# Kernel optimization log

Measured on AMD Instinct MI355X. Metric: run time of the kernel, lower is better.

## Reference

```python
import jax, jax.numpy as jnp
import numpy as np

C_Z = 128
C_S = 1024
C_S_OUT = 1024
B, L = 1, 1024


def setup_inputs() -> dict:
    key = jax.random.key(0)
    ks = jax.random.split(key, 8)
    s_z = jax.random.normal(ks[0], (B, L, L, C_Z), dtype=jnp.float32)
    s_s_in = jax.random.normal(ks[1], (B, L, C_S), dtype=jnp.float32)
    pair_mask = jnp.ones((B, L, L), dtype=jnp.float32)
    scale = 0.02
    return {
        "s_z": s_z,
        "s_s_in": s_s_in,
        "pair_mask": pair_mask,
        "ln_g": jnp.ones((C_Z,), jnp.float32),
        "ln_b": jnp.zeros((C_Z,), jnp.float32),
        "w1": jax.random.normal(ks[2], (C_Z, C_Z), jnp.float32) * scale,
        "b1": jnp.zeros((C_Z,), jnp.float32),
        "w2": jax.random.normal(ks[3], (C_Z, C_Z), jnp.float32) * scale,
        "b2": jnp.zeros((C_Z,), jnp.float32),
        "wc": jax.random.normal(ks[4], (C_S_OUT, 2 * C_Z + C_S), jnp.float32) * scale,
        "bc": jnp.zeros((C_S_OUT,), jnp.float32),
    }


def _layernorm(x, g, b, eps=1e-5):
    mu = jnp.mean(x, axis=-1, keepdims=True)
    var = jnp.mean(jnp.square(x - mu), axis=-1, keepdims=True)
    return (x - mu) * jax.lax.rsqrt(var + eps) * g + b


def reference(s_z, s_s_in, pair_mask, ln_g, ln_b, w1, b1, w2, b2, wc, bc):
    # LayerNorm -> Linear -> ReLU -> Linear over last dim (c_z)
    z = _layernorm(s_z, ln_g, ln_b)
    z = jax.nn.relu(jnp.einsum("blmc,dc->blmd", z, w1) + b1)
    z = jnp.einsum("blmc,dc->blmd", z, w2) + b2
    z = z * pair_mask[..., None]
    # masked mean over columns (dim=2) and rows (dim=1)
    norm_c = jnp.clip(jnp.sum(pair_mask, axis=2), 1.0, None)  # (B, L)
    s_s_c = jnp.sum(z, axis=2) / norm_c[..., None]            # (B, L, c_z)
    norm_r = jnp.clip(jnp.sum(pair_mask, axis=1), 1.0, None)
    s_s_r = jnp.sum(z, axis=1) / norm_r[..., None]
    cat = jnp.concatenate([s_s_c, s_s_r, s_s_in], axis=-1)    # (B, L, 2*c_z + c_s)
    return jnp.einsum("blc,dc->bld", cat, wc) + bc            # (B, L, c_s_out)
```

## Files before the change

kernel.cpp:

```cpp
#include <hip/hip_runtime.h>
#include <hip/hip_bf16.h>


typedef short bf16x8 __attribute__((ext_vector_type(8)));
typedef short short4v __attribute__((ext_vector_type(4)));
typedef float f32x16 __attribute__((ext_vector_type(16)));

static __device__ __forceinline__ short f2bf(float f) {
  unsigned u = __float_as_uint(f);
  u += 0x7fffu + ((u >> 16) & 1u);
  return (short)(u >> 16);
}
static __device__ __forceinline__ float bf2f(short s) {
  return __uint_as_float(((unsigned)(unsigned short)s) << 16);
}

__global__ __launch_bounds__(256, 2) void k_pair(
    const float* __restrict__ z, const float* __restrict__ pm,
    const float* __restrict__ lng, const float* __restrict__ lnb,
    const float* __restrict__ w1, const float* __restrict__ b1,
    float* __restrict__ g, float* __restrict__ gr,
    float* __restrict__ Mc, float* __restrict__ Mr)
{
  __shared__ __align__(16) short As[2][64 * 136];
  __shared__ float maskS[2][64];

  const int tid  = threadIdx.x;
  const int lane = tid & 63;
  const int wv   = tid >> 6;
  const int rt   = wv >> 1;
  const int ch   = wv & 1;
  const int ln   = lane & 31;
  const int hh   = lane >> 5;
  const int l0   = blockIdx.y * 32;
  const int m0   = blockIdx.x * 32;
  const int c8   = (tid & 15) * 8;

  float lg[8], lb[8];
  #pragma unroll
  for (int j = 0; j < 8; ++j) { lg[j] = lng[c8 + j]; lb[j] = lnb[c8 + j]; }

  float b1v[2];
  #pragma unroll
  for (int cc = 0; cc < 2; ++cc) b1v[cc] = b1[(ch * 2 + cc) * 32 + ln];

  bf16x8 bF[2][8];
  #pragma unroll
  for (int cc = 0; cc < 2; ++cc) {
    const int n = (ch * 2 + cc) * 32 + ln;
    #pragma unroll
    for (int k0 = 0; k0 < 8; ++k0) {
      const float* wp = w1 + n * 128 + k0 * 16 + hh * 8;
      float4 f0 = *(const float4*)wp;
      float4 f1 = *(const float4*)(wp + 4);
      bf16x8 t;
      t[0]=f2bf(f0.x); t[1]=f2bf(f0.y); t[2]=f2bf(f0.z); t[3]=f2bf(f0.w);
      t[4]=f2bf(f1.x); t[5]=f2bf(f1.y); t[6]=f2bf(f1.z); t[7]=f2bf(f1.w);
      bF[cc][k0] = t;
    }
  }

  float grA[2][16];
  #pragma unroll
  for (int cc = 0; cc < 2; ++cc)
    #pragma unroll
    for (int i = 0; i < 16; ++i) grA[cc][i] = 0.f;
  float mrAcc = 0.f;

  float4 xa[4], xb[4];
  float  mv = 0.f;
  auto LOADB = [&](int b) {
    #pragma unroll
    for (int p = 0; p < 4; ++p) {
      const int r = p * 16 + (tid >> 4);
      const int l = l0 + b * 2 + (r >> 5);
      const int m = m0 + (r & 31);
      const float* src = z + ((size_t)l * 1024 + (size_t)m) * 128 + c8;
      xa[p] = *(const float4*)src;
      xb[p] = *(const float4*)(src + 4);
    }
    if (tid < 64)
      mv = pm[(size_t)(l0 + b * 2 + (tid >> 5)) * 1024 + (m0 + (tid & 31))];
  };

  LOADB(0);

  #pragma unroll 1
  for (int b = 0; b < 16; ++b) {
    const int buf = b & 1;
    #pragma unroll
    for (int p = 0; p < 4; ++p) {
      const int r = p * 16 + (tid >> 4);
      float x[8] = {xa[p].x, xa[p].y, xa[p].z, xa[p].w,
                    xb[p].x, xb[p].y, xb[p].z, xb[p].w};
      float s = 0.f, s2 = 0.f;
      #pragma unroll
      for (int j = 0; j < 8; ++j) { s += x[j]; s2 += x[j] * x[j]; }
      #pragma unroll
      for (int off = 1; off < 16; off <<= 1) {
        s  += __shfl_xor(s, off);
        s2 += __shfl_xor(s2, off);
      }
      const float mu  = s * (1.f / 128.f);
      const float var = s2 * (1.f / 128.f) - mu * mu;
      const float rs  = rsqrtf(var + 1e-5f);
      bf16x8 o;
      #pragma unroll
      for (int j = 0; j < 8; ++j) o[j] = f2bf((x[j] - mu) * rs * lg[j] + lb[j]);
      *(bf16x8*)(&As[buf][r * 136 + c8]) = o;
    }
    if (tid < 64) maskS[buf][tid] = mv;
    __syncthreads();

    if (b < 15) LOADB(b + 1);

    f32x16 acc0, acc1;
    #pragma unroll
    for (int i = 0; i < 16; ++i) { acc0[i] = 0.f; acc1[i] = 0.f; }
    #pragma unroll
    for (int k0 = 0; k0 < 8; ++k0) {
      bf16x8 aF = *(bf16x8*)(&As[buf][(rt * 32 + ln) * 136 + k0 * 16 + hh * 8]);
      acc0 = __builtin_amdgcn_mfma_f32_32x32x16_bf16(aF, bF[0][k0], acc0, 0, 0, 0);
      acc1 = __builtin_amdgcn_mfma_f32_32x32x16_bf16(aF, bF[1][k0], acc1, 0, 0, 0);
    }

    float mrow[16];
    #pragma unroll
    for (int i = 0; i < 16; ++i) {
      const int cr = (i & 3) + 8 * (i >> 2) + 4 * hh;
      mrow[i] = maskS[buf][rt * 32 + cr];
    }
    const int lrow = l0 + b * 2 + rt;
    float s0 = 0.f, s1 = 0.f;
    #pragma unroll
    for (int i = 0; i < 16; ++i) {
      const float v0 = fmaxf(acc0[i] + b1v[0], 0.f) * mrow[i];
      const float v1 = fmaxf(acc1[i] + b1v[1], 0.f) * mrow[i];
      grA[0][i] += v0; grA[1][i] += v1;
      s0 += v0; s1 += v1;
    }
    s0 += __shfl_xor(s0, 32);
    s1 += __shfl_xor(s1, 32);
    if (lane < 32) {
      atomicAdd(&g[lrow * 128 + (ch * 2 + 0) * 32 + lane], s0);
      atomicAdd(&g[lrow * 128 + (ch * 2 + 1) * 32 + lane], s1);
    }

    if (wv == 0) {
      const float v = maskS[buf][lane];
      mrAcc += v;
      float rsum = v;
      #pragma unroll
      for (int off = 1; off < 32; off <<= 1) rsum += __shfl_xor(rsum, off);
      if (ln == 0) atomicAdd(&Mc[l0 + b * 2 + hh], rsum);
    }
  }

  if (wv == 0) {
    const float v = mrAcc + __shfl_xor(mrAcc, 32);
    if (lane < 32) atomicAdd(&Mr[m0 + lane], v);
  }

  __syncthreads();
  float* red1 = (float*)&As[0][0];
  if (rt == 1) {
    #pragma unroll
    for (int cc = 0; cc < 2; ++cc)
      #pragma unroll
      for (int i = 0; i < 16; ++i) {
        const int cr = (i & 3) + 8 * (i >> 2) + 4 * hh;
        red1[((ch * 2 + cc) * 32 + cr) * 32 + ln] = grA[cc][i];
      }
  }
  __syncthreads();
  if (rt == 0) {
    #pragma unroll
    for (int cc = 0; cc < 2; ++cc)
      #pragma unroll
      for (int i = 0; i < 16; ++i) {
        const int cr = (i & 3) + 8 * (i >> 2) + 4 * hh;
        const float v = grA[cc][i] + red1[((ch * 2 + cc) * 32 + cr) * 32 + ln];
        atomicAdd(&gr[(m0 + cr) * 128 + (ch * 2 + cc) * 32 + ln], v);
      }
  }
}

__global__ __launch_bounds__(256, 2) void k_seqproj(
    const float* __restrict__ gg, const float* __restrict__ w2,
    const float* __restrict__ b2, const float* __restrict__ Mc,
    const float* __restrict__ Mr, short* __restrict__ Ah, short* __restrict__ Al)
{
  __shared__ __align__(16) short As[64 * 136];
  __shared__ float Mvs[64];

  const int tid = threadIdx.x, lane = tid & 63, wv = tid >> 6;
  const int rt = wv >> 1, ch = wv & 1, ln = lane & 31, hh = lane >> 5;
  const int r0 = blockIdx.x * 64;
  const int c8 = (tid & 15) * 8;

  float b2v[2];
  #pragma unroll
  for (int cc = 0; cc < 2; ++cc) b2v[cc] = b2[(ch * 2 + cc) * 32 + ln];

  bf16x8 bF[2][8];
  #pragma unroll
  for (int cc = 0; cc < 2; ++cc) {
    const int n = (ch * 2 + cc) * 32 + ln;
    #pragma unroll
    for (int k0 = 0; k0 < 8; ++k0) {
      const float* wp = w2 + n * 128 + k0 * 16 + hh * 8;
      float4 f0 = *(const float4*)wp;
      float4 f1 = *(const float4*)(wp + 4);
      bf16x8 t;
      t[0]=f2bf(f0.x); t[1]=f2bf(f0.y); t[2]=f2bf(f0.z); t[3]=f2bf(f0.w);
      t[4]=f2bf(f1.x); t[5]=f2bf(f1.y); t[6]=f2bf(f1.z); t[7]=f2bf(f1.w);
      bF[cc][k0] = t;
    }
  }

  #pragma unroll
  for (int p = 0; p < 4; ++p) {
    const int r = p * 16 + (tid >> 4);
    const float* src = gg + (size_t)(r0 + r) * 128 + c8;
    float4 f0 = *(const float4*)src;
    float4 f1 = *(const float4*)(src + 4);
    bf16x8 o;
    o[0]=f2bf(f0.x); o[1]=f2bf(f0.y); o[2]=f2bf(f0.z); o[3]=f2bf(f0.w);
    o[4]=f2bf(f1.x); o[5]=f2bf(f1.y); o[6]=f2bf(f1.z); o[7]=f2bf(f1.w);
    *(bf16x8*)(&As[r * 136 + c8]) = o;
  }
  if (tid < 64) {
    const int p = r0 + tid;
    Mvs[tid] = (p < 1024) ? Mc[p] : Mr[p - 1024];
  }
  __syncthreads();

  f32x16 acc0, acc1;
  #pragma unroll
  for (int i = 0; i < 16; ++i) { acc0[i] = 0.f; acc1[i] = 0.f; }
  #pragma unroll
  for (int k0 = 0; k0 < 8; ++k0) {
    bf16x8 aF = *(bf16x8*)(&As[(rt * 32 + ln) * 136 + k0 * 16 + hh * 8]);
    acc0 = __builtin_amdgcn_mfma_f32_32x32x16_bf16(aF, bF[0][k0], acc0, 0, 0, 0);
    acc1 = __builtin_amdgcn_mfma_f32_32x32x16_bf16(aF, bF[1][k0], acc1, 0, 0, 0);
  }

  const int base = (r0 < 1024) ? 0 : 128;
  #pragma unroll
  for (int i = 0; i < 16; ++i) {
    const int cr = (i & 3) + 8 * (i >> 2) + 4 * hh;
    const int p = r0 + rt * 32 + cr;
    const int row = p & 1023;
    const float mvv = Mvs[rt * 32 + cr];
    const float dn = fmaxf(mvv, 1.f);
    const float v0 = (acc0[i] + b2v[0] * mvv) / dn;
    const float v1 = (acc1[i] + b2v[1] * mvv) / dn;
    const int c0 = base + (ch * 2 + 0) * 32 + ln;
    const int c1 = base + (ch * 2 + 1) * 32 + ln;
    const short h0 = f2bf(v0), h1 = f2bf(v1);
    Ah[(size_t)row * 1280 + c0] = h0;
    Al[(size_t)row * 1280 + c0] = f2bf(v0 - bf2f(h0));
    Ah[(size_t)row * 1280 + c1] = h1;
    Al[(size_t)row * 1280 + c1] = f2bf(v1 - bf2f(h1));
  }
}

__global__ void k_split(const float* __restrict__ s_in, const float* __restrict__ wc,
                        short* __restrict__ Ah, short* __restrict__ Al,
                        short* __restrict__ Bh, short* __restrict__ Bl)
{
  const int idx = blockIdx.x * 256 + threadIdx.x;

  if (idx < 262144) {
    const int row = idx >> 8;
    const int c4  = (idx & 255) * 4;
    float4 v = *(const float4*)(s_in + (size_t)row * 1024 + c4);
    float x[4] = {v.x, v.y, v.z, v.w};
    short4v hi, lo;
    #pragma unroll
    for (int j = 0; j < 4; ++j) {
      const short h = f2bf(x[j]);
      hi[j] = h; lo[j] = f2bf(x[j] - bf2f(h));
    }
    const size_t o = (size_t)row * 1280 + 256 + c4;
    *(short4v*)(Ah + o) = hi;
    *(short4v*)(Al + o) = lo;
  }
  if (idx < 327680) {
    const int row = idx / 320;
    const int c4  = (idx - row * 320) * 4;
    float4 v = *(const float4*)(wc + (size_t)row * 1280 + c4);
    float x[4] = {v.x, v.y, v.z, v.w};
    short4v hi, lo;
    #pragma unroll
    for (int j = 0; j < 4; ++j) {
      const short h = f2bf(x[j]);
      hi[j] = h; lo[j] = f2bf(x[j] - bf2f(h));
    }
    const size_t o = (size_t)row * 1280 + c4;
    *(short4v*)(Bh + o) = hi;
    *(short4v*)(Bl + o) = lo;
  }
}

__global__ __launch_bounds__(256, 2) void k_final(
    const short* __restrict__ Ah, const short* __restrict__ Al,
    const short* __restrict__ Bh, const short* __restrict__ Bl,
    const float* __restrict__ bc, float* __restrict__ out)
{
  __shared__ __align__(16) short sAh[64 * 40], sAl[64 * 40];
  __shared__ __align__(16) short sBh[64 * 40], sBl[64 * 40];
  const int tid = threadIdx.x, lane = tid & 63, wv = tid >> 6;
  const int mi = (wv >> 1) * 32, ni = (wv & 1) * 32;
  const int ln = lane & 31, hh = lane >> 5;
  const int m0 = blockIdx.y * 64, n0 = blockIdx.x * 64;
  const int rS = tid >> 2;
  const int kb = (tid & 3) * 8;

  const float bcv = bc[n0 + ni + ln];
  f32x16 acc;
  #pragma unroll
  for (int i = 0; i < 16; ++i) acc[i] = 0.f;

  bf16x8 rAh, rAl, rBh, rBl;
  auto LOADK = [&](int kk0) {
    rAh = *(const bf16x8*)(Ah + (size_t)(m0 + rS) * 1280 + kk0 + kb);
    rAl = *(const bf16x8*)(Al + (size_t)(m0 + rS) * 1280 + kk0 + kb);
    rBh = *(const bf16x8*)(Bh + (size_t)(n0 + rS) * 1280 + kk0 + kb);
    rBl = *(const bf16x8*)(Bl + (size_t)(n0 + rS) * 1280 + kk0 + kb);
  };
  LOADK(0);

  #pragma unroll 1
  for (int kk0 = 0; kk0 < 1280; kk0 += 32) {
    if (kk0) __syncthreads();
    *(bf16x8*)(sAh + rS * 40 + kb) = rAh;
    *(bf16x8*)(sAl + rS * 40 + kb) = rAl;
    *(bf16x8*)(sBh + rS * 40 + kb) = rBh;
    *(bf16x8*)(sBl + rS * 40 + kb) = rBl;
    __syncthreads();
    if (kk0 < 1280 - 32) LOADK(kk0 + 32);

    #pragma unroll
    for (int k0 = 0; k0 < 2; ++k0) {
      bf16x8 aH = *(bf16x8*)(sAh + (mi + ln) * 40 + k0 * 16 + hh * 8);
      bf16x8 aL = *(bf16x8*)(sAl + (mi + ln) * 40 + k0 * 16 + hh * 8);
      bf16x8 bH = *(bf16x8*)(sBh + (ni + ln) * 40 + k0 * 16 + hh * 8);
      bf16x8 bL = *(bf16x8*)(sBl + (ni + ln) * 40 + k0 * 16 + hh * 8);
      acc = __builtin_amdgcn_mfma_f32_32x32x16_bf16(aH, bH, acc, 0, 0, 0);
      acc = __builtin_amdgcn_mfma_f32_32x32x16_bf16(aH, bL, acc, 0, 0, 0);
      acc = __builtin_amdgcn_mfma_f32_32x32x16_bf16(aL, bH, acc, 0, 0, 0);
    }
  }

  #pragma unroll
  for (int i = 0; i < 16; ++i) {
    const int cr = (i & 3) + 8 * (i >> 2) + 4 * hh;
    out[(size_t)(m0 + mi + cr) * 1024 + n0 + ni + ln] = acc[i] + bcv;
  }
}

extern "C" void kernel_launch(void* const* d_in, const int* in_sizes, int n_in,
                              void* d_out, int out_size, void* d_ws, size_t ws_size,
                              hipStream_t stream) {
  const float* s_z    = (const float*)d_in[0];
  const float* s_s_in = (const float*)d_in[1];
  const float* pmask  = (const float*)d_in[2];
  const float* ln_g   = (const float*)d_in[3];
  const float* ln_b   = (const float*)d_in[4];
  const float* w1     = (const float*)d_in[5];
  const float* b1     = (const float*)d_in[6];
  const float* w2     = (const float*)d_in[7];
  const float* b2     = (const float*)d_in[8];
  const float* wc     = (const float*)d_in[9];
  const float* bc     = (const float*)d_in[10];
  float* outp = (float*)d_out;

  float* g  = (float*)d_ws;
  float* gr = g  + 1024 * 128;
  float* Mc = gr + 1024 * 128;
  float* Mr = Mc + 1024;
  short* Ah = (short*)(Mr + 1024);
  short* Al = Ah + (size_t)1024 * 1280;
  short* Bh = Al + (size_t)1024 * 1280;
  short* Bl = Bh + (size_t)1024 * 1280;

  hipMemsetAsync(d_ws, 0, (size_t)(2 * 1024 * 128 + 2048) * sizeof(float), stream);

  k_split<<<1280, 256, 0, stream>>>(s_s_in, wc, Ah, Al, Bh, Bl);
  k_pair<<<dim3(32, 32), 256, 0, stream>>>(s_z, pmask, ln_g, ln_b, w1, b1, g, gr, Mc, Mr);
  k_seqproj<<<32, 256, 0, stream>>>(g, w2, b2, Mc, Mr, Ah, Al);
  k_final<<<dim3(16, 16), 256, 0, stream>>>(Ah, Al, Bh, Bl, bc, outp);
}
```

Baseline: 764.2 us.

## Replace global atomic accumulation with per-block partial buffers and a reduce kernel

The pair kernel now writes its row and column partial sums into per-block slices of two large scratch buffers with plain stores, instead of doing atomicAdd into shared global accumulators. A new reduction kernel then sums the 32 partials for each output element. The memset shrinks to just the mask counters. This is meant to remove atomic contention and serialization, at the cost of about 32 MB of extra scratch traffic and an additional kernel launch.

```diff
diff --git a/kernel.cpp b/kernel.cpp
--- a/kernel.cpp
+++ b/kernel.cpp
@@ -19,7 +19,7 @@
     const float* __restrict__ z, const float* __restrict__ pm,
     const float* __restrict__ lng, const float* __restrict__ lnb,
     const float* __restrict__ w1, const float* __restrict__ b1,
-    float* __restrict__ g, float* __restrict__ gr,
+    float* __restrict__ gP, float* __restrict__ grP,
     float* __restrict__ Mc, float* __restrict__ Mr)
 {
   __shared__ __align__(16) short As[2][64 * 136];
@@ -32,8 +32,9 @@
   const int ch   = wv & 1;
   const int ln   = lane & 31;
   const int hh   = lane >> 5;
-  const int l0   = blockIdx.y * 32;
-  const int m0   = blockIdx.x * 32;
+  const int bx   = blockIdx.x, by = blockIdx.y;
+  const int l0   = by * 32;
+  const int m0   = bx * 32;
   const int c8   = (tid & 15) * 8;
 
   float lg[8], lb[8];
@@ -142,8 +143,9 @@
     s0 += __shfl_xor(s0, 32);
     s1 += __shfl_xor(s1, 32);
     if (lane < 32) {
-      atomicAdd(&g[lrow * 128 + (ch * 2 + 0) * 32 + lane], s0);
-      atomicAdd(&g[lrow * 128 + (ch * 2 + 1) * 32 + lane], s1);
+      float* dst = gP + ((size_t)bx * 1024 + lrow) * 128;
+      dst[(ch * 2 + 0) * 32 + lane] = s0;
+      dst[(ch * 2 + 1) * 32 + lane] = s1;
     }
 
     if (wv == 0) {
@@ -180,9 +182,28 @@
       for (int i = 0; i < 16; ++i) {
         const int cr = (i & 3) + 8 * (i >> 2) + 4 * hh;
         const float v = grA[cc][i] + red1[((ch * 2 + cc) * 32 + cr) * 32 + ln];
-        atomicAdd(&gr[(m0 + cr) * 128 + (ch * 2 + cc) * 32 + ln], v);
+        grP[((size_t)by * 1024 + (m0 + cr)) * 128 + (ch * 2 + cc) * 32 + ln] = v;
       }
   }
+}
+
+__global__ void k_reduce(const float* __restrict__ gP, const float* __restrict__ grP,
+                         float* __restrict__ g, float* __restrict__ gr)
+{
+  const int idx = blockIdx.x * 256 + threadIdx.x;
+  const bool isG = idx < 32768;
+  const int t = isG ? idx : idx - 32768;
+  const float* src = isG ? gP : grP;
+  float* dst = isG ? g : gr;
+  const int row = t >> 5;
+  const int c4  = (t & 31) * 4;
+  float4 s = {0.f, 0.f, 0.f, 0.f};
+  #pragma unroll 8
+  for (int x = 0; x < 32; ++x) {
+    float4 v = *(const float4*)(src + ((size_t)x * 1024 + row) * 128 + c4);
+    s.x += v.x; s.y += v.y; s.z += v.z; s.w += v.w;
+  }
+  *(float4*)(dst + (size_t)row * 128 + c4) = s;
 }
 
 __global__ __launch_bounds__(256, 2) void k_seqproj(
@@ -376,19 +397,22 @@
   const float* bc     = (const float*)d_in[10];
   float* outp = (float*)d_out;
 
-  float* g  = (float*)d_ws;
-  float* gr = g  + 1024 * 128;
-  float* Mc = gr + 1024 * 128;
-  float* Mr = Mc + 1024;
-  short* Ah = (short*)(Mr + 1024);
-  short* Al = Ah + (size_t)1024 * 1280;
-  short* Bh = Al + (size_t)1024 * 1280;
-  short* Bl = Bh + (size_t)1024 * 1280;
-
-  hipMemsetAsync(d_ws, 0, (size_t)(2 * 1024 * 128 + 2048) * sizeof(float), stream);
+  float* Mc  = (float*)d_ws;
+  float* Mr  = Mc + 1024;
+  float* g   = Mr + 1024;
+  float* gr  = g  + 131072;
+  float* gP  = gr + 131072;
+  float* grP = gP + 4194304;
+  short* Ah  = (short*)(grP + 4194304);
+  short* Al  = Ah + (size_t)1024 * 1280;
+  short* Bh  = Al + (size_t)1024 * 1280;
+  short* Bl  = Bh + (size_t)1024 * 1280;
+
+  hipMemsetAsync(d_ws, 0, 2048 * sizeof(float), stream);
 
   k_split<<<1280, 256, 0, stream>>>(s_s_in, wc, Ah, Al, Bh, Bl);
-  k_pair<<<dim3(32, 32), 256, 0, stream>>>(s_z, pmask, ln_g, ln_b, w1, b1, g, gr, Mc, Mr);
+  k_pair<<<dim3(32, 32), 256, 0, stream>>>(s_z, pmask, ln_g, ln_b, w1, b1, gP, grP, Mc, Mr);
+  k_reduce<<<256, 256, 0, stream>>>(gP, grP, g, gr);
   k_seqproj<<<32, 256, 0, stream>>>(g, w2, b2, Mc, Mr, Ah, Al);
   k_final<<<dim3(16, 16), 256, 0, stream>>>(Ah, Al, Bh, Bl, bc, outp);
 }
```

Measured after the change: 771.9 us. Within noise of the previous version (+1.0%).
